# Kernel optimization log

Measured on AMD Instinct MI355X. Metric: run time of the kernel, lower is better.

The kernel has to match this reference:

```python
import jax, jax.numpy as jnp
import numpy as np

VOCAB = 32000
EMBED = 300
HIDDEN = 1150
LAYER_SIZES = [EMBED, HIDDEN, HIDDEN, EMBED]  # in->out per LSTM layer
SCALE = EMBED ** 0.5


def _lstm_layer(x, W_ih, W_hh, b_ih, b_hh):
    """Single-layer batch-first LSTM, zero initial state.
    x: [B,S,D]; W_ih: [4H,D]; W_hh: [4H,H]; biases: [4H].
    PyTorch gate order: i, f, g, o.
    Returns outputs [B,S,H]."""
    B = x.shape[0]
    H = W_hh.shape[1]
    # Precompute input contribution for all timesteps: [S,B,4H]
    x_gates = jnp.einsum('bsd,gd->sbg', x, W_ih) + (b_ih + b_hh)

    def step(carry, xg):
        h, c = carry
        gates = xg + h @ W_hh.T  # [B,4H]
        i, f, g, o = jnp.split(gates, 4, axis=-1)
        i = jax.nn.sigmoid(i)
        f = jax.nn.sigmoid(f)
        g = jnp.tanh(g)
        o = jax.nn.sigmoid(o)
        c = f * c + i * g
        h = o * jnp.tanh(c)
        return (h, c), h

    h0 = jnp.zeros((B, H), dtype=x.dtype)
    c0 = jnp.zeros((B, H), dtype=x.dtype)
    _, hs = jax.lax.scan(step, (h0, c0), x_gates)  # hs: [S,B,H]
    return hs.transpose(1, 0, 2)


def setup_inputs() -> dict:
    key = jax.random.key(0)
    ks = jax.random.split(key, 16)
    inp = {}
    inp['input_ids'] = jax.random.randint(ks[0], (16, 256), 0, VOCAB, dtype=jnp.int32)
    emb = jax.random.uniform(ks[1], (VOCAB, EMBED), dtype=jnp.float32, minval=-0.1, maxval=0.1)
    emb = emb.at[0].set(0.0)  # padding_idx = 0
    inp['embedding'] = emb
    k = 2
    for l in range(3):
        din, dout = LAYER_SIZES[l], LAYER_SIZES[l + 1]
        inp[f'W_ih{l}'] = jax.random.normal(ks[k], (4 * dout, din), dtype=jnp.float32) * (1.0 / np.sqrt(din)); k += 1
        inp[f'W_hh{l}'] = jax.random.normal(ks[k], (4 * dout, dout), dtype=jnp.float32) * (1.0 / np.sqrt(dout)); k += 1
        b_ih = jnp.zeros((4 * dout,), dtype=jnp.float32)
        b_ih = b_ih.at[dout:2 * dout].set(1.0)  # forget-gate bias = 1
        inp[f'b_ih{l}'] = b_ih
        inp[f'b_hh{l}'] = jnp.zeros((4 * dout,), dtype=jnp.float32)
    return inp


def reference(input_ids, embedding,
              W_ih0, W_hh0, b_ih0, b_hh0,
              W_ih1, W_hh1, b_ih1, b_hh1,
              W_ih2, W_hh2, b_ih2, b_hh2):
    # Eval-mode AWD-LSTM forward: all dropouts are identity; scale applied.
    x = embedding[input_ids] * SCALE  # [B,S,E]
    x = _lstm_layer(x, W_ih0, W_hh0, b_ih0, b_hh0)  # [B,S,H]
    x = _lstm_layer(x, W_ih1, W_hh1, b_ih1, b_hh1)  # [B,S,H]
    x = _lstm_layer(x, W_ih2, W_hh2, b_ih2, b_hh2)  # [B,S,E]
    # Tied output projection: Linear(E -> V, bias=False) with weight = embedding
    logits = jnp.einsum('bse,ve->bsv', x, embedding)
    return logits
```

## Files before the change

### kernel.cpp

```cpp
#include <hip/hip_runtime.h>

#define BB 16
#define SS 256
#define NVOCAB 32000
#define NEMB 300

#define CHUNK 6
#define NT 384
#define NSTR 384

typedef float f4_t __attribute__((ext_vector_type(4)));
typedef unsigned int u4_t __attribute__((ext_vector_type(4)));
typedef short bf16x8 __attribute__((ext_vector_type(8)));
typedef float f32x4 __attribute__((ext_vector_type(4)));
typedef unsigned short ushort_t;

__device__ __forceinline__ f4_t load_f4u(const float* p) {
    f4_t v;
    __builtin_memcpy(&v, p, sizeof(f4_t));
    return v;
}

__device__ __forceinline__ void llc_store_u4_drain(u4_t* p, u4_t v) {
    asm volatile("global_store_dwordx4 %0, %1, off sc0 sc1\n\t"
                 "s_waitcnt vmcnt(0)" :: "v"(p), "v"(v) : "memory");
}

__device__ __forceinline__ void llc_load8_wait(
        u4_t& u0, u4_t& u1, u4_t& u2, u4_t& u3,
        u4_t& u4v, u4_t& u5v, u4_t& u6v, u4_t& u7v,
        const u4_t* p0, const u4_t* p1, const u4_t* p2, const u4_t* p3,
        const u4_t* p4, const u4_t* p5, const u4_t* p6, const u4_t* p7) {
    asm volatile(
        "global_load_dwordx4 %0, %8, off sc0 sc1\n\t"
        "global_load_dwordx4 %1, %9, off sc0 sc1\n\t"
        "global_load_dwordx4 %2, %10, off sc0 sc1\n\t"
        "global_load_dwordx4 %3, %11, off sc0 sc1\n\t"
        "global_load_dwordx4 %4, %12, off sc0 sc1\n\t"
        "global_load_dwordx4 %5, %13, off sc0 sc1\n\t"
        "global_load_dwordx4 %6, %14, off sc0 sc1\n\t"
        "global_load_dwordx4 %7, %15, off sc0 sc1\n\t"
        "s_waitcnt vmcnt(0)"
        : "=&v"(u0), "=&v"(u1), "=&v"(u2), "=&v"(u3),
          "=&v"(u4v), "=&v"(u5v), "=&v"(u6v), "=&v"(u7v)
        : "v"(p0), "v"(p1), "v"(p2), "v"(p3),
          "v"(p4), "v"(p5), "v"(p6), "v"(p7)
        : "memory");
}

__global__ void embed_kernel(const int* __restrict__ ids,
                             const float* __restrict__ emb,
                             float* __restrict__ x0) {
    int bs = blockIdx.x;
    int id = ids[bs];
    const float* row = emb + (size_t)id * NEMB;
    float* out = x0 + (size_t)bs * NEMB;
    const float scale = 17.320508075688772f;
    for (int e = threadIdx.x; e < NEMB; e += blockDim.x)
        out[e] = row[e] * scale;
}

__global__ void conv_split(const float* __restrict__ src,
                           ushort_t* __restrict__ hi, ushort_t* __restrict__ lo,
                           int N, int K, int KP, int total) {
    for (int i = blockIdx.x * blockDim.x + threadIdx.x; i < total;
         i += gridDim.x * blockDim.x) {
        int r = i / KP, k = i - r * KP;
        float v = (r < N && k < K) ? src[(size_t)r * K + k] : 0.f;
        unsigned u = __float_as_uint(v);
        unsigned hb = (u + 0x7FFFu + ((u >> 16) & 1u)) >> 16;
        float hf = __uint_as_float(hb << 16);
        float rem = v - hf;
        unsigned u2 = __float_as_uint(rem);
        unsigned lb = (u2 + 0x7FFFu + ((u2 >> 16) & 1u)) >> 16;
        hi[i] = (ushort_t)hb;
        lo[i] = (ushort_t)lb;
    }
}

__global__ __launch_bounds__(256) void gemm_mfma(
        const ushort_t* __restrict__ Ah, const ushort_t* __restrict__ Al,
        const ushort_t* __restrict__ Wh, const ushort_t* __restrict__ Wl,
        float* __restrict__ C, int N, int KP,
        const float* __restrict__ bias_i, const float* __restrict__ bias_h,
        int permuted) {
    constexpr int LD = 40;
    __shared__ ushort_t sA[2][128 * LD];
    __shared__ ushort_t sW[2][128 * LD];
    const int t    = threadIdx.x;
    const int lane = t & 63;
    const int wave = t >> 6;
    const int wm   = wave >> 1, wn = wave & 1;
    const int n0   = blockIdx.x * 128;
    const int m0   = blockIdx.y * 128;

    f32x4 acc[4][4];
    #pragma unroll
    for (int i = 0; i < 4; i++)
        #pragma unroll
        for (int j = 0; j < 4; j++)
            acc[i][j] = (f32x4){0.f, 0.f, 0.f, 0.f};

    const int nkt = KP >> 5;
    for (int kt = 0; kt < nkt; kt++) {
        __syncthreads();
        #pragma unroll
        for (int c = 0; c < 2; c++) {
            int id = t + c * 256;
            int r = id >> 2, kq = id & 3;
            int so = r * LD + kq * 8;
            size_t goA = (size_t)(m0 + r) * KP + kt * 32 + kq * 8;
            size_t goW = (size_t)(n0 + r) * KP + kt * 32 + kq * 8;
            *reinterpret_cast<u4_t*>(&sA[0][so]) = *reinterpret_cast<const u4_t*>(Ah + goA);
            *reinterpret_cast<u4_t*>(&sA[1][so]) = *reinterpret_cast<const u4_t*>(Al + goA);
            *reinterpret_cast<u4_t*>(&sW[0][so]) = *reinterpret_cast<const u4_t*>(Wh + goW);
            *reinterpret_cast<u4_t*>(&sW[1][so]) = *reinterpret_cast<const u4_t*>(Wl + goW);
        }
        __syncthreads();

        bf16x8 ah[4], al[4], wh[4], wl[4];
        #pragma unroll
        for (int i = 0; i < 4; i++) {
            int ro = (wm * 64 + i * 16 + (lane & 15)) * LD + (lane >> 4) * 8;
            int co = (wn * 64 + i * 16 + (lane & 15)) * LD + (lane >> 4) * 8;
            ah[i] = *reinterpret_cast<const bf16x8*>(&sA[0][ro]);
            al[i] = *reinterpret_cast<const bf16x8*>(&sA[1][ro]);
            wh[i] = *reinterpret_cast<const bf16x8*>(&sW[0][co]);
            wl[i] = *reinterpret_cast<const bf16x8*>(&sW[1][co]);
        }
        #pragma unroll
        for (int i = 0; i < 4; i++)
            #pragma unroll
            for (int j = 0; j < 4; j++) {
                acc[i][j] = __builtin_amdgcn_mfma_f32_16x16x32_bf16(ah[i], wh[j], acc[i][j], 0, 0, 0);
                acc[i][j] = __builtin_amdgcn_mfma_f32_16x16x32_bf16(ah[i], wl[j], acc[i][j], 0, 0, 0);
                acc[i][j] = __builtin_amdgcn_mfma_f32_16x16x32_bf16(al[i], wh[j], acc[i][j], 0, 0, 0);
            }
    }

    #pragma unroll
    for (int i = 0; i < 4; i++) {
        int row = m0 + wm * 64 + i * 16 + ((lane >> 4) << 2);
        #pragma unroll
        for (int j = 0; j < 4; j++) {
            int col = n0 + wn * 64 + j * 16 + (lane & 15);
            if (col < N) {
                float bv = bias_i ? (bias_i[col] + bias_h[col]) : 0.f;
                #pragma unroll
                for (int r2 = 0; r2 < 4; r2++) {
                    int m = row + r2;
                    float v = acc[i][j][r2] + bv;
                    size_t idx;
                    if (permuted) {
                        int b_ = m >> 8;
                        int s_ = m & 255;
                        idx = ((size_t)s_ * BB + b_) * (size_t)N + col;
                    } else {
                        idx = (size_t)m * (size_t)N + col;
                    }
                    C[idx] = v;
                }
            }
        }
    }
}

template<int SW, int NCHR>
__global__ __launch_bounds__(NT, 1) void lstm_rec(
        const float* __restrict__ Whh,
        const float* __restrict__ xg,
        float* __restrict__ xout,
        u4_t* __restrict__ hx,
        int H, unsigned TB) {
    constexpr int KP   = 48 * SW;
    constexpr int LDH  = KP + 4;
    constexpr int NSUB = SW / 8;
    constexpr int PRS  = 17;
    constexpr int PSS  = 24 * PRS + 4;
    extern __shared__ __align__(16) float lds[];
    float* ht   = lds;
    float* pbuf = ht + 16 * LDH;
    float* gbuf = pbuf + 24 * PSS;
    float* cbuf = gbuf + NT;
    float* hlx  = cbuf + 96;

    const int t    = threadIdx.x;
    const int lane = t & 63;
    const int wv   = t >> 6;
    const int ks   = t >> 3;
    const int rg   = t & 7;
    const int h0   = blockIdx.x * CHUNK;
    const int G4   = 4 * H;

    const float* wr[3];
    #pragma unroll
    for (int j = 0; j < 3; j++) {
        int r = 3 * rg + j, g = r / CHUNK, l = r - g * CHUNK;
        int grow = ((h0 + l) < H) ? (g * H + h0 + l) : 0;
        wr[j] = Whh + (size_t)grow * (size_t)H;
    }

    for (int i = t; i < 16 * LDH; i += NT) ht[i] = 0.f;
    if (t < 96) cbuf[t] = 0.f;
    __syncthreads();

    const int r_row = t >> 4, r_b = t & 15;
    const int r_g = r_row / CHUNK, r_l = r_row - r_g * CHUNK;
    const int r_h = ((h0 + r_l) < H) ? (h0 + r_l) : h0;
    const float* xgp = xg + (size_t)r_b * G4 + (size_t)r_g * H + r_h;

    const int pairidx = (lane >> 4) & 3;
    const int prow3   = 3 * (lane & 7);

    #pragma unroll 1
    for (int s = 0; s < SS; s++) {
        const u4_t* hcb = hx + (size_t)(s & 1) * (16 * NSTR);
        u4_t*       hpb = hx + (size_t)((s + 1) & 1) * (16 * NSTR);
        const unsigned tgt = TB + (unsigned)s;
        float xgv = xgp[(size_t)s * (size_t)(16 * G4)];

        if (s > 0 && t < NCHR) {
            const u4_t* cb = hcb + t;
            #pragma unroll
            for (int rh = 0; rh < 2; rh++) {
                const u4_t* q0 = cb + (rh * 8 + 0) * NSTR;
                const u4_t* q1 = cb + (rh * 8 + 1) * NSTR;
                const u4_t* q2 = cb + (rh * 8 + 2) * NSTR;
                const u4_t* q3 = cb + (rh * 8 + 3) * NSTR;
                const u4_t* q4 = cb + (rh * 8 + 4) * NSTR;
                const u4_t* q5 = cb + (rh * 8 + 5) * NSTR;
                const u4_t* q6 = cb + (rh * 8 + 6) * NSTR;
                const u4_t* q7 = cb + (rh * 8 + 7) * NSTR;
                u4_t u0, u1, u2, u3, u4v, u5v, u6v, u7v;
                for (;;) {
                    llc_load8_wait(u0, u1, u2, u3, u4v, u5v, u6v, u7v,
                                   q0, q1, q2, q3, q4, q5, q6, q7);
                    int ok = (u0.w >= tgt) & (u1.w >= tgt) & (u2.w >= tgt) & (u3.w >= tgt)
                           & (u4v.w >= tgt) & (u5v.w >= tgt) & (u6v.w >= tgt) & (u7v.w >= tgt);
                    if (ok) break;
                }
                float* d;
                d = ht + (rh * 8 + 0) * LDH + 3 * t;
                d[0] = __uint_as_float(u0.x); d[1] = __uint_as_float(u0.y); d[2] = __uint_as_float(u0.z);
                d = ht + (rh * 8 + 1) * LDH + 3 * t;
                d[0] = __uint_as_float(u1.x); d[1] = __uint_as_float(u1.y); d[2] = __uint_as_float(u1.z);
                d = ht + (rh * 8 + 2) * LDH + 3 * t;
                d[0] = __uint_as_float(u2.x); d[1] = __uint_as_float(u2.y); d[2] = __uint_as_float(u2.z);
                d = ht + (rh * 8 + 3) * LDH + 3 * t;
                d[0] = __uint_as_float(u3.x); d[1] = __uint_as_float(u3.y); d[2] = __uint_as_float(u3.z);
                d = ht + (rh * 8 + 4) * LDH + 3 * t;
                d[0] = __uint_as_float(u4v.x); d[1] = __uint_as_float(u4v.y); d[2] = __uint_as_float(u4v.z);
                d = ht + (rh * 8 + 5) * LDH + 3 * t;
                d[0] = __uint_as_float(u5v.x); d[1] = __uint_as_float(u5v.y); d[2] = __uint_as_float(u5v.z);
                d = ht + (rh * 8 + 6) * LDH + 3 * t;
                d[0] = __uint_as_float(u6v.x); d[1] = __uint_as_float(u6v.y); d[2] = __uint_as_float(u6v.z);
                d = ht + (rh * 8 + 7) * LDH + 3 * t;
                d[0] = __uint_as_float(u7v.x); d[1] = __uint_as_float(u7v.y); d[2] = __uint_as_float(u7v.z);
            }
        }
        __syncthreads();

        float a[3][16];
        #pragma unroll
        for (int j = 0; j < 3; j++)
            #pragma unroll
            for (int b = 0; b < 16; b++) a[j][b] = 0.f;

        if (s > 0) {
            #pragma unroll
            for (int sub = 0; sub < NSUB; sub++) {
                const int kk = ks * SW + sub * 8;
                const int k0 = (kk < H) ? kk : 0;
                const int k1 = (kk + 4 < H) ? (kk + 4) : 0;
                const f4_t w00 = load_f4u(wr[0] + k0), w01 = load_f4u(wr[0] + k1);
                const f4_t w10 = load_f4u(wr[1] + k0), w11 = load_f4u(wr[1] + k1);
                const f4_t w20 = load_f4u(wr[2] + k0), w21 = load_f4u(wr[2] + k1);
                const float* hb = ht + kk;
                #pragma unroll
                for (int b = 0; b < 16; b++) {
                    const f4_t h0v = *reinterpret_cast<const f4_t*>(hb + b * LDH);
                    const f4_t h1v = *reinterpret_cast<const f4_t*>(hb + b * LDH + 4);
                    float acc;
                    acc = a[0][b];
                    acc = fmaf(w00.x, h0v.x, acc); acc = fmaf(w00.y, h0v.y, acc);
                    acc = fmaf(w00.z, h0v.z, acc); acc = fmaf(w00.w, h0v.w, acc);
                    acc = fmaf(w01.x, h1v.x, acc); acc = fmaf(w01.y, h1v.y, acc);
                    acc = fmaf(w01.z, h1v.z, acc); acc = fmaf(w01.w, h1v.w, acc);
                    a[0][b] = acc;
                    acc = a[1][b];
                    acc = fmaf(w10.x, h0v.x, acc); acc = fmaf(w10.y, h0v.y, acc);
                    acc = fmaf(w10.z, h0v.z, acc); acc = fmaf(w10.w, h0v.w, acc);
                    acc = fmaf(w11.x, h1v.x, acc); acc = fmaf(w11.y, h1v.y, acc);
                    acc = fmaf(w11.z, h1v.z, acc); acc = fmaf(w11.w, h1v.w, acc);
                    a[1][b] = acc;
                    acc = a[2][b];
                    acc = fmaf(w20.x, h0v.x, acc); acc = fmaf(w20.y, h0v.y, acc);
                    acc = fmaf(w20.z, h0v.z, acc); acc = fmaf(w20.w, h0v.w, acc);
                    acc = fmaf(w21.x, h1v.x, acc); acc = fmaf(w21.y, h1v.y, acc);
                    acc = fmaf(w21.z, h1v.z, acc); acc = fmaf(w21.w, h1v.w, acc);
                    a[2][b] = acc;
                }
            }
        }

        #pragma unroll
        for (int j = 0; j < 3; j++)
            #pragma unroll
            for (int b = 0; b < 16; b++) {
                float v = a[j][b] + __shfl_xor(a[j][b], 8);
                if ((lane & 8) == 0)
                    pbuf[(wv * 4 + pairidx) * PSS + (prow3 + j) * PRS + b] = v;
            }
        __syncthreads();

        {
            float dot = xgv;
            #pragma unroll
            for (int q = 0; q < 24; q++)
                dot += pbuf[q * PSS + r_row * PRS + r_b];
            gbuf[t] = dot;
        }
        __syncthreads();

        if (t < 96) {
            int l = t >> 4, b = t & 15;
            float gi = gbuf[(0 * CHUNK + l) * 16 + b];
            float gf = gbuf[(1 * CHUNK + l) * 16 + b];
            float gg = gbuf[(2 * CHUNK + l) * 16 + b];
            float go = gbuf[(3 * CHUNK + l) * 16 + b];
            float iv = 1.f / (1.f + expf(-gi));
            float fv = 1.f / (1.f + expf(-gf));
            float gv = tanhf(gg);
            float ov = 1.f / (1.f + expf(-go));
            float c  = fv * cbuf[t] + iv * gv;
            cbuf[t]  = c;
            float hv = ov * tanhf(c);
            hv = ((h0 + l) < H) ? hv : 0.f;
            hlx[b * CHUNK + l] = hv;
            if ((h0 + l) < H)
                xout[(size_t)b * ((size_t)SS * H) + (size_t)s * H + (h0 + l)] = hv;
        }
        __syncthreads();

        if (t < 32) {
            int bq = t >> 1, cj = t & 1;
            u4_t pk;
            pk.x = __float_as_uint(hlx[bq * CHUNK + 3 * cj + 0]);
            pk.y = __float_as_uint(hlx[bq * CHUNK + 3 * cj + 1]);
            pk.z = __float_as_uint(hlx[bq * CHUNK + 3 * cj + 2]);
            pk.w = tgt + 1u;
            llc_store_u4_drain(hpb + bq * NSTR + (h0 / 3 + cj), pk);
        }
    }
}

extern "C" void kernel_launch(void* const* d_in, const int* in_sizes, int n_in,
                              void* d_out, int out_size, void* d_ws, size_t ws_size,
                              hipStream_t stream) {
    const int*   ids  = (const int*)d_in[0];
    const float* emb  = (const float*)d_in[1];
    const float* Wih0 = (const float*)d_in[2];
    const float* Whh0 = (const float*)d_in[3];
    const float* bih0 = (const float*)d_in[4];
    const float* bhh0 = (const float*)d_in[5];
    const float* Wih1 = (const float*)d_in[6];
    const float* Whh1 = (const float*)d_in[7];
    const float* bih1 = (const float*)d_in[8];
    const float* bhh1 = (const float*)d_in[9];
    const float* Wih2 = (const float*)d_in[10];
    const float* Whh2 = (const float*)d_in[11];
    const float* bih2 = (const float*)d_in[12];
    const float* bhh2 = (const float*)d_in[13];
    float* out = (float*)d_out;

    float* ws = (float*)d_ws;
    float* xA = ws;
    float* xB = xA + 1228800;
    float* xg = xB + 4710400;
    u4_t*  hx = (u4_t*)(xg + 18841600);
    (void)in_sizes; (void)n_in; (void)out_size; (void)ws_size;

    ushort_t* sc  = (ushort_t*)d_out;
    ushort_t* tAh = sc;
    ushort_t* tAl = tAh + (size_t)4096 * 1152;
    ushort_t* W0h = tAl + (size_t)4096 * 1152;
    ushort_t* W0l = W0h + (size_t)4608 * 320;
    ushort_t* W1h = W0l + (size_t)4608 * 320;
    ushort_t* W1l = W1h + (size_t)4608 * 1152;
    ushort_t* W2h = W1l + (size_t)4608 * 1152;
    ushort_t* W2l = W2h + (size_t)1280 * 1152;

    ushort_t* fAh = (ushort_t*)xB;
    ushort_t* fAl = fAh + (size_t)4096 * 320;
    ushort_t* fWh = (ushort_t*)xg;
    ushort_t* fWl = fWh + (size_t)32000 * 320;

    hipMemsetAsync(hx, 0, (size_t)2 * 16 * NSTR * 16, stream);

    const size_t lds01 = (size_t)(16 * 1156 + 24 * 412 + NT + 96 + 96) * 4;
    const size_t lds2  = (size_t)(16 * 388  + 24 * 412 + NT + 96 + 96) * 4;

    conv_split<<<dim3(720), dim3(256), 0, stream>>>(Wih0, W0h, W0l, 4600, 300, 320, 4608 * 320);
    conv_split<<<dim3(2048), dim3(256), 0, stream>>>(Wih1, W1h, W1l, 4600, 1150, 1152, 4608 * 1152);
    conv_split<<<dim3(720), dim3(256), 0, stream>>>(Wih2, W2h, W2l, 1200, 1150, 1152, 1280 * 1152);

    embed_kernel<<<dim3(BB * SS), dim3(256), 0, stream>>>(ids, emb, xA);

    conv_split<<<dim3(640), dim3(256), 0, stream>>>(xA, tAh, tAl, 4096, 300, 320, 4096 * 320);
    gemm_mfma<<<dim3(36, 32), dim3(256), 0, stream>>>(tAh, tAl, W0h, W0l, xg,
                                                      4600, 320, bih0, bhh0, 1);
    lstm_rec<24, 384><<<dim3(192), dim3(NT), lds01, stream>>>(Whh0, xg, xB, hx, 1150, 0u);

    conv_split<<<dim3(2048), dim3(256), 0, stream>>>(xB, tAh, tAl, 4096, 1150, 1152, 4096 * 1152);
    gemm_mfma<<<dim3(36, 32), dim3(256), 0, stream>>>(tAh, tAl, W1h, W1l, xg,
                                                      4600, 1152, bih1, bhh1, 1);
    lstm_rec<24, 384><<<dim3(192), dim3(NT), lds01, stream>>>(Whh1, xg, xB, hx, 1150, 256u);

    conv_split<<<dim3(2048), dim3(256), 0, stream>>>(xB, tAh, tAl, 4096, 1150, 1152, 4096 * 1152);
    gemm_mfma<<<dim3(10, 32), dim3(256), 0, stream>>>(tAh, tAl, W2h, W2l, xg,
                                                      1200, 1152, bih2, bhh2, 1);
    lstm_rec<8, 100><<<dim3(50), dim3(NT), lds2, stream>>>(Whh2, xg, xA, hx, 300, 512u);

    conv_split<<<dim3(640), dim3(256), 0, stream>>>(xA, fAh, fAl, 4096, 300, 320, 4096 * 320);
    conv_split<<<dim3(2048), dim3(256), 0, stream>>>(emb, fWh, fWl, 32000, 300, 320, 32000 * 320);

    gemm_mfma<<<dim3(250, 32), dim3(256), 0, stream>>>(fAh, fAl, fWh, fWl, out,
                                                       NVOCAB, 320, nullptr, nullptr, 0);
}
```

Measured before the change: 8.438 ms.

## Add LDS-resident-weight LSTM recurrence kernel for layer 0

Adds a new recurrent kernel that keeps each block's slice of W_hh (24 rows by 1152) in shared memory for the whole sequence instead of streaming it each step. Each step is split into two half-batch passes of 8 sequences, so the h buffer in LDS is smaller and the second half's wait on the flag-tagged hidden state overlaps with the first half's compute. Only layer 0 uses the new kernel. The cost is extra LDS (about 160 KB), two more barriers per step, and per-thread weight reloads from LDS in each half.

```diff
diff --git a/kernel.cpp b/kernel.cpp
--- a/kernel.cpp
+++ b/kernel.cpp
@@ -161,6 +161,268 @@
                     C[idx] = v;
                 }
             }
+        }
+    }
+}
+
+__global__ __launch_bounds__(NT, 1) void lstm_recW(
+        const float* __restrict__ Whh,
+        const float* __restrict__ xg,
+        float* __restrict__ xout,
+        u4_t* __restrict__ hx,
+        int H, unsigned TB) {
+    constexpr int LDH = 1156;
+    constexpr int PRS = 17;
+    constexpr int PSS = 24 * PRS + 4;
+    extern __shared__ __align__(16) float lds[];
+    float* wp   = lds;
+    float* ht   = wp + 27648;
+    float* pbuf = ht + 9248;
+    float* gbuf = pbuf + 6 * PSS;
+    float* cbuf = gbuf + NT;
+    float* hlx  = cbuf + 96;
+
+    const int t    = threadIdx.x;
+    const int lane = t & 63;
+    const int wv   = t >> 6;
+    const int ks   = t >> 3;
+    const int rg   = t & 7;
+    const int h0   = blockIdx.x * CHUNK;
+    const int G4   = 4 * H;
+
+    f4_t* wp4 = reinterpret_cast<f4_t*>(wp);
+
+    #pragma unroll
+    for (int j = 0; j < 3; j++) {
+        int r = 3 * rg + j, g = r / CHUNK, l = r - g * CHUNK;
+        bool okr = (h0 + l) < H;
+        const float* src = Whh + (size_t)(okr ? (g * H + h0 + l) : 0) * (size_t)H;
+        #pragma unroll
+        for (int sub = 0; sub < 3; sub++)
+            #pragma unroll
+            for (int q = 0; q < 2; q++) {
+                int k = ks * 24 + sub * 8 + q * 4;
+                f4_t v; v.x = 0.f; v.y = 0.f; v.z = 0.f; v.w = 0.f;
+                if (okr) {
+                    if (k + 0 < H) v.x = src[k + 0];
+                    if (k + 1 < H) v.y = src[k + 1];
+                    if (k + 2 < H) v.z = src[k + 2];
+                    if (k + 3 < H) v.w = src[k + 3];
+                }
+                wp4[((j * 3 + sub) * 2 + q) * NT + t] = v;
+            }
+    }
+    for (int i = t; i < 8 * LDH; i += NT) ht[i] = 0.f;
+    if (t < 96) cbuf[t] = 0.f;
+    __syncthreads();
+
+    const int r_row = t >> 4, r_b = t & 15;
+    const int r_g = r_row / CHUNK, r_l = r_row - r_g * CHUNK;
+    const int r_h = ((h0 + r_l) < H) ? (h0 + r_l) : h0;
+    const float* xgp = xg + (size_t)r_b * G4 + (size_t)r_g * H + r_h;
+    const int prow3 = 3 * rg;
+
+    #pragma unroll 1
+    for (int s = 0; s < SS; s++) {
+        const u4_t* hcb = hx + (size_t)(s & 1) * (16 * NSTR);
+        u4_t*       hpb = hx + (size_t)((s + 1) & 1) * (16 * NSTR);
+        const unsigned tgt = TB + (unsigned)s;
+        float xgv = xgp[(size_t)s * (size_t)(16 * G4)];
+        const u4_t* cb = hcb + t;
+
+        if (s > 0) {
+            u4_t u0, u1, u2, u3, u4v, u5v, u6v, u7v;
+            for (;;) {
+                llc_load8_wait(u0, u1, u2, u3, u4v, u5v, u6v, u7v,
+                               cb + 0 * NSTR, cb + 1 * NSTR, cb + 2 * NSTR, cb + 3 * NSTR,
+                               cb + 4 * NSTR, cb + 5 * NSTR, cb + 6 * NSTR, cb + 7 * NSTR);
+                int ok = (u0.w >= tgt) & (u1.w >= tgt) & (u2.w >= tgt) & (u3.w >= tgt)
+                       & (u4v.w >= tgt) & (u5v.w >= tgt) & (u6v.w >= tgt) & (u7v.w >= tgt);
+                if (ok) break;
+            }
+            float* d;
+            d = ht + 0 * LDH + 3 * t; d[0] = __uint_as_float(u0.x);  d[1] = __uint_as_float(u0.y);  d[2] = __uint_as_float(u0.z);
+            d = ht + 1 * LDH + 3 * t; d[0] = __uint_as_float(u1.x);  d[1] = __uint_as_float(u1.y);  d[2] = __uint_as_float(u1.z);
+            d = ht + 2 * LDH + 3 * t; d[0] = __uint_as_float(u2.x);  d[1] = __uint_as_float(u2.y);  d[2] = __uint_as_float(u2.z);
+            d = ht + 3 * LDH + 3 * t; d[0] = __uint_as_float(u3.x);  d[1] = __uint_as_float(u3.y);  d[2] = __uint_as_float(u3.z);
+            d = ht + 4 * LDH + 3 * t; d[0] = __uint_as_float(u4v.x); d[1] = __uint_as_float(u4v.y); d[2] = __uint_as_float(u4v.z);
+            d = ht + 5 * LDH + 3 * t; d[0] = __uint_as_float(u5v.x); d[1] = __uint_as_float(u5v.y); d[2] = __uint_as_float(u5v.z);
+            d = ht + 6 * LDH + 3 * t; d[0] = __uint_as_float(u6v.x); d[1] = __uint_as_float(u6v.y); d[2] = __uint_as_float(u6v.z);
+            d = ht + 7 * LDH + 3 * t; d[0] = __uint_as_float(u7v.x); d[1] = __uint_as_float(u7v.y); d[2] = __uint_as_float(u7v.z);
+        }
+        __syncthreads();
+
+        {
+            float a[3][8];
+            #pragma unroll
+            for (int j = 0; j < 3; j++)
+                #pragma unroll
+                for (int b = 0; b < 8; b++) a[j][b] = 0.f;
+            if (s > 0) {
+                #pragma unroll
+                for (int sub = 0; sub < 3; sub++) {
+                    const f4_t w00 = wp4[((0 * 3 + sub) * 2 + 0) * NT + t];
+                    const f4_t w01 = wp4[((0 * 3 + sub) * 2 + 1) * NT + t];
+                    const f4_t w10 = wp4[((1 * 3 + sub) * 2 + 0) * NT + t];
+                    const f4_t w11 = wp4[((1 * 3 + sub) * 2 + 1) * NT + t];
+                    const f4_t w20 = wp4[((2 * 3 + sub) * 2 + 0) * NT + t];
+                    const f4_t w21 = wp4[((2 * 3 + sub) * 2 + 1) * NT + t];
+                    const float* hb = ht + ks * 24 + sub * 8;
+                    #pragma unroll
+                    for (int b = 0; b < 8; b++) {
+                        const f4_t h0v = *reinterpret_cast<const f4_t*>(hb + b * LDH);
+                        const f4_t h1v = *reinterpret_cast<const f4_t*>(hb + b * LDH + 4);
+                        float acc;
+                        acc = a[0][b];
+                        acc = fmaf(w00.x, h0v.x, acc); acc = fmaf(w00.y, h0v.y, acc);
+                        acc = fmaf(w00.z, h0v.z, acc); acc = fmaf(w00.w, h0v.w, acc);
+                        acc = fmaf(w01.x, h1v.x, acc); acc = fmaf(w01.y, h1v.y, acc);
+                        acc = fmaf(w01.z, h1v.z, acc); acc = fmaf(w01.w, h1v.w, acc);
+                        a[0][b] = acc;
+                        acc = a[1][b];
+                        acc = fmaf(w10.x, h0v.x, acc); acc = fmaf(w10.y, h0v.y, acc);
+                        acc = fmaf(w10.z, h0v.z, acc); acc = fmaf(w10.w, h0v.w, acc);
+                        acc = fmaf(w11.x, h1v.x, acc); acc = fmaf(w11.y, h1v.y, acc);
+                        acc = fmaf(w11.z, h1v.z, acc); acc = fmaf(w11.w, h1v.w, acc);
+                        a[1][b] = acc;
+                        acc = a[2][b];
+                        acc = fmaf(w20.x, h0v.x, acc); acc = fmaf(w20.y, h0v.y, acc);
+                        acc = fmaf(w20.z, h0v.z, acc); acc = fmaf(w20.w, h0v.w, acc);
+                        acc = fmaf(w21.x, h1v.x, acc); acc = fmaf(w21.y, h1v.y, acc);
+                        acc = fmaf(w21.z, h1v.z, acc); acc = fmaf(w21.w, h1v.w, acc);
+                        a[2][b] = acc;
+                    }
+                }
+            }
+            #pragma unroll
+            for (int j = 0; j < 3; j++)
+                #pragma unroll
+                for (int b = 0; b < 8; b++) {
+                    float v = a[j][b];
+                    v += __shfl_xor(v, 8);
+                    v += __shfl_xor(v, 16);
+                    v += __shfl_xor(v, 32);
+                    if (lane < 8)
+                        pbuf[wv * PSS + (prow3 + j) * PRS + b] = v;
+                }
+        }
+        __syncthreads();
+
+        if (s > 0) {
+            u4_t u0, u1, u2, u3, u4v, u5v, u6v, u7v;
+            for (;;) {
+                llc_load8_wait(u0, u1, u2, u3, u4v, u5v, u6v, u7v,
+                               cb + 8 * NSTR, cb + 9 * NSTR, cb + 10 * NSTR, cb + 11 * NSTR,
+                               cb + 12 * NSTR, cb + 13 * NSTR, cb + 14 * NSTR, cb + 15 * NSTR);
+                int ok = (u0.w >= tgt) & (u1.w >= tgt) & (u2.w >= tgt) & (u3.w >= tgt)
+                       & (u4v.w >= tgt) & (u5v.w >= tgt) & (u6v.w >= tgt) & (u7v.w >= tgt);
+                if (ok) break;
+            }
+            float* d;
+            d = ht + 0 * LDH + 3 * t; d[0] = __uint_as_float(u0.x);  d[1] = __uint_as_float(u0.y);  d[2] = __uint_as_float(u0.z);
+            d = ht + 1 * LDH + 3 * t; d[0] = __uint_as_float(u1.x);  d[1] = __uint_as_float(u1.y);  d[2] = __uint_as_float(u1.z);
+            d = ht + 2 * LDH + 3 * t; d[0] = __uint_as_float(u2.x);  d[1] = __uint_as_float(u2.y);  d[2] = __uint_as_float(u2.z);
+            d = ht + 3 * LDH + 3 * t; d[0] = __uint_as_float(u3.x);  d[1] = __uint_as_float(u3.y);  d[2] = __uint_as_float(u3.z);
+            d = ht + 4 * LDH + 3 * t; d[0] = __uint_as_float(u4v.x); d[1] = __uint_as_float(u4v.y); d[2] = __uint_as_float(u4v.z);
+            d = ht + 5 * LDH + 3 * t; d[0] = __uint_as_float(u5v.x); d[1] = __uint_as_float(u5v.y); d[2] = __uint_as_float(u5v.z);
+            d = ht + 6 * LDH + 3 * t; d[0] = __uint_as_float(u6v.x); d[1] = __uint_as_float(u6v.y); d[2] = __uint_as_float(u6v.z);
+            d = ht + 7 * LDH + 3 * t; d[0] = __uint_as_float(u7v.x); d[1] = __uint_as_float(u7v.y); d[2] = __uint_as_float(u7v.z);
+        }
+        __syncthreads();
+
+        {
+            float a[3][8];
+            #pragma unroll
+            for (int j = 0; j < 3; j++)
+                #pragma unroll
+                for (int b = 0; b < 8; b++) a[j][b] = 0.f;
+            if (s > 0) {
+                #pragma unroll
+                for (int sub = 0; sub < 3; sub++) {
+                    const f4_t w00 = wp4[((0 * 3 + sub) * 2 + 0) * NT + t];
+                    const f4_t w01 = wp4[((0 * 3 + sub) * 2 + 1) * NT + t];
+                    const f4_t w10 = wp4[((1 * 3 + sub) * 2 + 0) * NT + t];
+                    const f4_t w11 = wp4[((1 * 3 + sub) * 2 + 1) * NT + t];
+                    const f4_t w20 = wp4[((2 * 3 + sub) * 2 + 0) * NT + t];
+                    const f4_t w21 = wp4[((2 * 3 + sub) * 2 + 1) * NT + t];
+                    const float* hb = ht + ks * 24 + sub * 8;
+                    #pragma unroll
+                    for (int b = 0; b < 8; b++) {
+                        const f4_t h0v = *reinterpret_cast<const f4_t*>(hb + b * LDH);
+                        const f4_t h1v = *reinterpret_cast<const f4_t*>(hb + b * LDH + 4);
+                        float acc;
+                        acc = a[0][b];
+                        acc = fmaf(w00.x, h0v.x, acc); acc = fmaf(w00.y, h0v.y, acc);
+                        acc = fmaf(w00.z, h0v.z, acc); acc = fmaf(w00.w, h0v.w, acc);
+                        acc = fmaf(w01.x, h1v.x, acc); acc = fmaf(w01.y, h1v.y, acc);
+                        acc = fmaf(w01.z, h1v.z, acc); acc = fmaf(w01.w, h1v.w, acc);
+                        a[0][b] = acc;
+                        acc = a[1][b];
+                        acc = fmaf(w10.x, h0v.x, acc); acc = fmaf(w10.y, h0v.y, acc);
+                        acc = fmaf(w10.z, h0v.z, acc); acc = fmaf(w10.w, h0v.w, acc);
+                        acc = fmaf(w11.x, h1v.x, acc); acc = fmaf(w11.y, h1v.y, acc);
+                        acc = fmaf(w11.z, h1v.z, acc); acc = fmaf(w11.w, h1v.w, acc);
+                        a[1][b] = acc;
+                        acc = a[2][b];
+                        acc = fmaf(w20.x, h0v.x, acc); acc = fmaf(w20.y, h0v.y, acc);
+                        acc = fmaf(w20.z, h0v.z, acc); acc = fmaf(w20.w, h0v.w, acc);
+                        acc = fmaf(w21.x, h1v.x, acc); acc = fmaf(w21.y, h1v.y, acc);
+                        acc = fmaf(w21.z, h1v.z, acc); acc = fmaf(w21.w, h1v.w, acc);
+                        a[2][b] = acc;
+                    }
+                }
+            }
+            #pragma unroll
+            for (int j = 0; j < 3; j++)
+                #pragma unroll
+                for (int b = 0; b < 8; b++) {
+                    float v = a[j][b];
+                    v += __shfl_xor(v, 8);
+                    v += __shfl_xor(v, 16);
+                    v += __shfl_xor(v, 32);
+                    if (lane < 8)
+                        pbuf[wv * PSS + (prow3 + j) * PRS + (b + 8)] = v;
+                }
+        }
+        __syncthreads();
+
+        {
+            float dot = xgv;
+            #pragma unroll
+            for (int wq = 0; wq < 6; wq++)
+                dot += pbuf[wq * PSS + r_row * PRS + r_b];
+            gbuf[t] = dot;
+        }
+        __syncthreads();
+
+        if (t < 96) {
+            int l = t >> 4, b = t & 15;
+            float gi = gbuf[(0 * CHUNK + l) * 16 + b];
+            float gf = gbuf[(1 * CHUNK + l) * 16 + b];
+            float gg = gbuf[(2 * CHUNK + l) * 16 + b];
+            float go = gbuf[(3 * CHUNK + l) * 16 + b];
+            float iv = 1.f / (1.f + expf(-gi));
+            float fv = 1.f / (1.f + expf(-gf));
+            float gv = tanhf(gg);
+            float ov = 1.f / (1.f + expf(-go));
+            float c  = fv * cbuf[t] + iv * gv;
+            cbuf[t]  = c;
+            float hv = ov * tanhf(c);
+            hv = ((h0 + l) < H) ? hv : 0.f;
+            hlx[b * CHUNK + l] = hv;
+            if ((h0 + l) < H)
+                xout[(size_t)b * ((size_t)SS * H) + (size_t)s * H + (h0 + l)] = hv;
+        }
+        __syncthreads();
+
+        if (t < 32) {
+            int bq = t >> 1, cj = t & 1;
+            u4_t pk;
+            pk.x = __float_as_uint(hlx[bq * CHUNK + 3 * cj + 0]);
+            pk.y = __float_as_uint(hlx[bq * CHUNK + 3 * cj + 1]);
+            pk.z = __float_as_uint(hlx[bq * CHUNK + 3 * cj + 2]);
+            pk.w = tgt + 1u;
+            llc_store_u4_drain(hpb + bq * NSTR + (h0 / 3 + cj), pk);
         }
     }
 }
@@ -397,6 +659,7 @@
 
     hipMemsetAsync(hx, 0, (size_t)2 * 16 * NSTR * 16, stream);
 
+    const size_t ldsW  = (size_t)(27648 + 9248 + 6 * 412 + NT + 96 + 96) * 4;
     const size_t lds01 = (size_t)(16 * 1156 + 24 * 412 + NT + 96 + 96) * 4;
     const size_t lds2  = (size_t)(16 * 388  + 24 * 412 + NT + 96 + 96) * 4;
 
@@ -409,7 +672,7 @@
     conv_split<<<dim3(640), dim3(256), 0, stream>>>(xA, tAh, tAl, 4096, 300, 320, 4096 * 320);
     gemm_mfma<<<dim3(36, 32), dim3(256), 0, stream>>>(tAh, tAl, W0h, W0l, xg,
                                                       4600, 320, bih0, bhh0, 1);
-    lstm_rec<24, 384><<<dim3(192), dim3(NT), lds01, stream>>>(Whh0, xg, xB, hx, 1150, 0u);
+    lstm_recW<<<dim3(192), dim3(NT), ldsW, stream>>>(Whh0, xg, xB, hx, 1150, 0u);
 
     conv_split<<<dim3(2048), dim3(256), 0, stream>>>(xB, tAh, tAl, 4096, 1150, 1152, 4096 * 1152);
     gemm_mfma<<<dim3(36, 32), dim3(256), 0, stream>>>(tAh, tAl, W1h, W1l, xg,
```

After: 8.509 ms. About the same (+0.8%).
